# Kernel tuning notes

Hardware: AMD Instinct MI355X
Metric: run time of the kernel (lower is better)

The kernel has to match this reference:

```python
import jax, jax.numpy as jnp
import numpy as np

V, H, L, B = 32000, 1024, 2, 64
TEMP = 0.8


def setup_inputs() -> dict:
    key = jax.random.key(0)
    ks = jax.random.split(key, 12)
    sV = 1.0 / np.sqrt(V)
    sH = 1.0 / np.sqrt(H)
    return {
        "x": jax.random.normal(ks[0], (B, V), jnp.float32),
        "hidden_states": jax.random.normal(ks[1], (L, B, H), jnp.float32),
        "cell_states": jax.random.normal(ks[2], (L, B, H), jnp.float32),
        # gate order along axis 1: f, i, o, g
        "Wh": jax.random.uniform(ks[3], (L, 4, H, H), jnp.float32, -sH, sH),
        "bh": jax.random.uniform(ks[4], (L, 4, H), jnp.float32, -sH, sH),
        "Wx0": jax.random.uniform(ks[5], (4, H, V), jnp.float32, -sV, sV),
        "bx0": jax.random.uniform(ks[6], (4, H), jnp.float32, -sV, sV),
        "Wx1": jax.random.uniform(ks[7], (4, H, H), jnp.float32, -sH, sH),
        "bx1": jax.random.uniform(ks[8], (4, H), jnp.float32, -sH, sH),
        "Wdec": jax.random.uniform(ks[9], (V, H), jnp.float32, -sH, sH),
        "bdec": jax.random.uniform(ks[10], (V,), jnp.float32, -sH, sH),
    }


def _lstm_cell(inp, h, c, Wx, bx, Whl, bhl):
    # fused gate pre-activations: [B, 4, H]
    z = (jnp.einsum("ghk,bk->bgh", Wx, inp) + bx[None]
         + jnp.einsum("ghk,bk->bgh", Whl, h) + bhl[None])
    f = jax.nn.sigmoid(z[:, 0])
    i = jax.nn.sigmoid(z[:, 1])
    o = jax.nn.sigmoid(z[:, 2])
    g = jnp.tanh(z[:, 3])
    c_new = f * c + i * g
    out = o * jnp.tanh(c_new)
    return out, c_new


def reference(x, hidden_states, cell_states, Wh, bh, Wx0, bx0, Wx1, bx1, Wdec, bdec):
    wx = [(Wx0, bx0), (Wx1, bx1)]
    outputs, cstates = [], []
    inp = x
    for l in range(L):
        out, c_new = _lstm_cell(inp, hidden_states[l], cell_states[l],
                                wx[l][0], wx[l][1], Wh[l], bh[l])
        outputs.append(out)
        cstates.append(c_new)
        inp = out
    logits = outputs[-1] @ Wdec.T + bdec
    logp = jax.nn.log_softmax(logits / TEMP, axis=-1)
    return logp, jnp.stack(outputs), jnp.stack(cstates)
```

## Files before the change

### kernel.cpp

```cpp
#include <hip/hip_runtime.h>
#include <hip/hip_bf16.h>
#include <cstdint>

#define DI __device__ __forceinline__

typedef __attribute__((ext_vector_type(8))) short short8;
typedef __attribute__((ext_vector_type(4))) float f32x4;
typedef __attribute__((ext_vector_type(4))) int int4v;

DI f32x4 mfma16(short8 a, short8 b, f32x4 c) {
  return __builtin_amdgcn_mfma_f32_16x16x32_bf16(a, b, c, 0, 0, 0);
}

DI uint32_t f2bf(float f) {
  uint32_t u = __float_as_uint(f);
  return (u + 0x7fffu + ((u >> 16) & 1u)) >> 16;
}

DI uint32_t pk2(float a, float b) {
  return f2bf(a) | (f2bf(b) << 16);
}

DI short8 cvt8(float4 a, float4 b) {
  int4v t;
  t.x = (int)pk2(a.x, a.y);
  t.y = (int)pk2(a.z, a.w);
  t.z = (int)pk2(b.x, b.y);
  t.w = (int)pk2(b.z, b.w);
  return __builtin_bit_cast(short8, t);
}

__global__ __launch_bounds__(256) void convert_k(
    const float* __restrict__ x, const float* __restrict__ hs,
    ushort* __restrict__ xb, ushort* __restrict__ hb) {
  const int NX4 = 512000;
  const int NH4 = 32768;
  int i = blockIdx.x * 256 + threadIdx.x;
  if (i < NX4) {
    float4 v = *(const float4*)(x + 4 * (size_t)i);
    uint2 o;
    o.x = pk2(v.x, v.y);
    o.y = pk2(v.z, v.w);
    *(uint2*)(xb + 4 * (size_t)i) = o;
  } else if (i < NX4 + NH4) {
    int j = i - NX4;
    float4 v = *(const float4*)(hs + 4 * (size_t)j);
    uint2 o;
    o.x = pk2(v.x, v.y);
    o.y = pk2(v.z, v.w);
    *(uint2*)(hb + 4 * (size_t)j) = o;
  }
}

__global__ __launch_bounds__(256) void gemm_gates(
    const ushort* __restrict__ A1, const float* __restrict__ W1, int K1, int nch1, int steps1,
    const ushort* __restrict__ A2, const float* __restrict__ W2, int K2, int nch2, int steps2,
    float* __restrict__ zpart) {
  const int hblk = blockIdx.x;
  const int chunk = blockIdx.y;
  const ushort* A;
  const float* W;
  int K, steps;
  long kbase;
  if (chunk < nch1) {
    A = A1; W = W1; K = K1; steps = steps1;
    kbase = (long)chunk * steps1 * 32;
  } else {
    A = A2; W = W2; K = K2; steps = steps2;
    kbase = (long)(chunk - nch1) * steps2 * 32;
  }
  const int tid = threadIdx.x;
  const int wv = tid >> 6;
  const int lane = tid & 63;
  const int l15 = lane & 15;
  const int l4 = lane >> 4;
  const int h = hblk * 64 + wv * 16 + l15;

  const ushort* arow[4];
#pragma unroll
  for (int m = 0; m < 4; ++m)
    arow[m] = A + (size_t)(m * 16 + l15) * K + kbase + l4 * 8;
  const float* wrow[4];
#pragma unroll
  for (int g = 0; g < 4; ++g)
    wrow[g] = W + (size_t)(g * 1024 + h) * K + kbase + l4 * 8;

  f32x4 acc[4][4];
#pragma unroll
  for (int g = 0; g < 4; ++g)
#pragma unroll
    for (int m = 0; m < 4; ++m)
      acc[g][m] = f32x4{0.f, 0.f, 0.f, 0.f};

  for (int s = 0; s < steps; ++s) {
    short8 af[4];
#pragma unroll
    for (int m = 0; m < 4; ++m)
      af[m] = *(const short8*)(arow[m] + (size_t)s * 32);
#pragma unroll
    for (int g = 0; g < 4; ++g) {
      const float* wp = wrow[g] + (size_t)s * 32;
      float4 w0 = *(const float4*)wp;
      float4 w1 = *(const float4*)(wp + 4);
      short8 bfr = cvt8(w0, w1);
#pragma unroll
      for (int m = 0; m < 4; ++m)
        acc[g][m] = mfma16(af[m], bfr, acc[g][m]);
    }
  }

  float* zp = zpart + (size_t)chunk * (64 * 4096) + (size_t)(l4 * 4) * 4096 + h;
#pragma unroll
  for (int g = 0; g < 4; ++g)
#pragma unroll
    for (int m = 0; m < 4; ++m)
#pragma unroll
      for (int r = 0; r < 4; ++r)
        zp[(size_t)(m * 16 + r) * 4096 + g * 1024] = acc[g][m][r];
}

__global__ __launch_bounds__(256) void lstm_cell_k(
    const float* __restrict__ zpart, int nslots,
    const float* __restrict__ bx, const float* __restrict__ bhl,
    const float* __restrict__ c_in,
    float* __restrict__ h_out, float* __restrict__ c_out,
    ushort* __restrict__ h_out_b) {
  int idx = blockIdx.x * 256 + threadIdx.x;
  if (idx >= 64 * 1024) return;
  int h = idx & 1023;
  float z0 = bx[h] + bhl[h];
  float z1 = bx[1024 + h] + bhl[1024 + h];
  float z2 = bx[2048 + h] + bhl[2048 + h];
  float z3 = bx[3072 + h] + bhl[3072 + h];
  int b = idx >> 10;
  const float* zp = zpart + (size_t)b * 4096 + h;
  for (int s = 0; s < nslots; ++s) {
    const float* p = zp + (size_t)s * (64 * 4096);
    z0 += p[0];
    z1 += p[1024];
    z2 += p[2048];
    z3 += p[3072];
  }
  float f = 1.f / (1.f + expf(-z0));
  float i = 1.f / (1.f + expf(-z1));
  float o = 1.f / (1.f + expf(-z2));
  float g = tanhf(z3);
  float c = f * c_in[idx] + i * g;
  float hv = o * tanhf(c);
  h_out[idx] = hv;
  c_out[idx] = c;
  h_out_b[idx] = (ushort)f2bf(hv);
}

__global__ __launch_bounds__(256) void gemm_dec(
    const ushort* __restrict__ A, const float* __restrict__ W,
    const float* __restrict__ bias, float* __restrict__ logits) {
  const int nblk = blockIdx.x;
  const int tid = threadIdx.x;
  const int wv = tid >> 6;
  const int lane = tid & 63;
  const int l15 = lane & 15;
  const int l4 = lane >> 4;
  const int col = nblk * 64 + wv * 16 + l15;

  const ushort* arow[4];
#pragma unroll
  for (int m = 0; m < 4; ++m)
    arow[m] = A + (size_t)(m * 16 + l15) * 1024 + l4 * 8;
  const float* wrow = W + (size_t)col * 1024 + l4 * 8;

  f32x4 acc[4];
#pragma unroll
  for (int m = 0; m < 4; ++m) acc[m] = f32x4{0.f, 0.f, 0.f, 0.f};

  for (int s = 0; s < 32; ++s) {
    short8 af[4];
#pragma unroll
    for (int m = 0; m < 4; ++m)
      af[m] = *(const short8*)(arow[m] + (size_t)s * 32);
    const float* wp = wrow + (size_t)s * 32;
    float4 w0 = *(const float4*)wp;
    float4 w1 = *(const float4*)(wp + 4);
    short8 bfr = cvt8(w0, w1);
#pragma unroll
    for (int m = 0; m < 4; ++m)
      acc[m] = mfma16(af[m], bfr, acc[m]);
  }

  float bv = bias[col];
  float* lp = logits + (size_t)(l4 * 4) * 32000 + col;
#pragma unroll
  for (int m = 0; m < 4; ++m)
#pragma unroll
    for (int r = 0; r < 4; ++r)
      lp[(size_t)(m * 16 + r) * 32000] = acc[m][r] + bv;
}

__global__ __launch_bounds__(256) void softmax_k(
    const float* __restrict__ logits, float* __restrict__ logp) {
  const int b = blockIdx.x;
  const int tid = threadIdx.x;
  const int wv = tid >> 6;
  const int lane = tid & 63;
  const float* row = logits + (size_t)b * 32000;
  __shared__ float rbuf[4];

  float m = -1e30f;
  for (int i = tid; i < 32000; i += 256) m = fmaxf(m, row[i]);
#pragma unroll
  for (int d = 1; d < 64; d <<= 1) m = fmaxf(m, __shfl_xor(m, d));
  if (lane == 0) rbuf[wv] = m;
  __syncthreads();
  m = fmaxf(fmaxf(rbuf[0], rbuf[1]), fmaxf(rbuf[2], rbuf[3]));
  __syncthreads();

  float sum = 0.f;
  for (int i = tid; i < 32000; i += 256) sum += expf((row[i] - m) * 1.25f);
#pragma unroll
  for (int d = 1; d < 64; d <<= 1) sum += __shfl_xor(sum, d);
  if (lane == 0) rbuf[wv] = sum;
  __syncthreads();
  sum = rbuf[0] + rbuf[1] + rbuf[2] + rbuf[3];
  float lse = logf(sum);

  float* op = logp + (size_t)b * 32000;
  for (int i = tid; i < 32000; i += 256)
    op[i] = (row[i] - m) * 1.25f - lse;
}

extern "C" void kernel_launch(void* const* d_in, const int* in_sizes, int n_in,
                              void* d_out, int out_size, void* d_ws, size_t ws_size,
                              hipStream_t stream) {
  const float* x    = (const float*)d_in[0];
  const float* hs   = (const float*)d_in[1];
  const float* cs   = (const float*)d_in[2];
  const float* Wh   = (const float*)d_in[3];
  const float* bh   = (const float*)d_in[4];
  const float* Wx0  = (const float*)d_in[5];
  const float* bx0  = (const float*)d_in[6];
  const float* Wx1  = (const float*)d_in[7];
  const float* bx1  = (const float*)d_in[8];
  const float* Wdec = (const float*)d_in[9];
  const float* bdec = (const float*)d_in[10];

  float* out   = (float*)d_out;
  float* logp  = out;
  float* houts = out + 2048000;
  float* couts = out + 2179072;

  char* ws = (char*)d_ws;
  ushort* xb     = (ushort*)ws;
  ushort* hb     = (ushort*)(ws + 4096000);
  ushort* outb   = (ushort*)(ws + 4096000 + 262144);
  float*  logits = (float*)(ws + 4096000 + 262144 + 262144);
  float*  zpart  = (float*)(ws + 4096000 + 262144 + 262144 + 8192000);
  const size_t fixed = 4096000ull + 262144 + 262144 + 8192000;
  const size_t slot = (size_t)64 * 4096 * 4;

  int nch1 = 20, steps1 = 50;
  int l1ch = 8, l1steps = 4;
  if (fixed + 24 * slot > ws_size) {
    nch1 = 10; steps1 = 100;
    if (fixed + 16 * slot > ws_size) {
      nch1 = 4; steps1 = 250;
      l1ch = 4; l1steps = 8;
    }
  }

  convert_k<<<2128, 256, 0, stream>>>(x, hs, xb, hb);

  gemm_gates<<<dim3(16, nch1 + 4), 256, 0, stream>>>(
      xb, Wx0, 32000, nch1, steps1,
      hb, Wh, 1024, 4, 8, zpart);

  lstm_cell_k<<<256, 256, 0, stream>>>(zpart, nch1 + 4, bx0, bh, cs,
                                       houts, couts, outb);

  gemm_gates<<<dim3(16, 2 * l1ch), 256, 0, stream>>>(
      outb, Wx1, 1024, l1ch, l1steps,
      hb + 65536, Wh + 4194304, 1024, l1ch, l1steps, zpart);

  lstm_cell_k<<<256, 256, 0, stream>>>(zpart, 2 * l1ch, bx1, bh + 4096,
                                       cs + 65536, houts + 65536, couts + 65536,
                                       outb + 65536);

  gemm_dec<<<500, 256, 0, stream>>>(outb + 65536, Wdec, bdec, logits);

  softmax_k<<<64, 256, 0, stream>>>(logits, logp);
}
```

Before: 314.4 us.

## Split gate GEMM over gate axis, shrink decoder blocks, two-pass split softmax

The gate GEMM now launches one block per gate via a z grid dimension, so each block keeps a quarter of the accumulators. The layer-0 K-split also goes from 20 to 25 chunks. The decoder GEMM uses 64-thread blocks with four times as many blocks. The single-block-per-row softmax becomes two kernels: per-chunk max/sum partials, then a combine and write pass spread over more blocks. The aim is more parallelism and occupancy on the many CUs, at the cost of an extra launch, re-reading the logits, and reloading the A fragments once per gate.

```diff
diff --git a/kernel.cpp b/kernel.cpp
--- a/kernel.cpp
+++ b/kernel.cpp
@@ -58,6 +58,7 @@
     float* __restrict__ zpart) {
   const int hblk = blockIdx.x;
   const int chunk = blockIdx.y;
+  const int g = blockIdx.z;
   const ushort* A;
   const float* W;
   int K, steps;
@@ -80,43 +81,33 @@
 #pragma unroll
   for (int m = 0; m < 4; ++m)
     arow[m] = A + (size_t)(m * 16 + l15) * K + kbase + l4 * 8;
-  const float* wrow[4];
-#pragma unroll
-  for (int g = 0; g < 4; ++g)
-    wrow[g] = W + (size_t)(g * 1024 + h) * K + kbase + l4 * 8;
-
-  f32x4 acc[4][4];
-#pragma unroll
-  for (int g = 0; g < 4; ++g)
-#pragma unroll
-    for (int m = 0; m < 4; ++m)
-      acc[g][m] = f32x4{0.f, 0.f, 0.f, 0.f};
+  const float* wrow = W + (size_t)(g * 1024 + h) * K + kbase + l4 * 8;
+
+  f32x4 acc[4];
+#pragma unroll
+  for (int m = 0; m < 4; ++m) acc[m] = f32x4{0.f, 0.f, 0.f, 0.f};
 
   for (int s = 0; s < steps; ++s) {
     short8 af[4];
 #pragma unroll
     for (int m = 0; m < 4; ++m)
       af[m] = *(const short8*)(arow[m] + (size_t)s * 32);
-#pragma unroll
-    for (int g = 0; g < 4; ++g) {
-      const float* wp = wrow[g] + (size_t)s * 32;
-      float4 w0 = *(const float4*)wp;
-      float4 w1 = *(const float4*)(wp + 4);
-      short8 bfr = cvt8(w0, w1);
-#pragma unroll
-      for (int m = 0; m < 4; ++m)
-        acc[g][m] = mfma16(af[m], bfr, acc[g][m]);
-    }
-  }
-
-  float* zp = zpart + (size_t)chunk * (64 * 4096) + (size_t)(l4 * 4) * 4096 + h;
-#pragma unroll
-  for (int g = 0; g < 4; ++g)
-#pragma unroll
-    for (int m = 0; m < 4; ++m)
-#pragma unroll
-      for (int r = 0; r < 4; ++r)
-        zp[(size_t)(m * 16 + r) * 4096 + g * 1024] = acc[g][m][r];
+    const float* wp = wrow + (size_t)s * 32;
+    float4 w0 = *(const float4*)wp;
+    float4 w1 = *(const float4*)(wp + 4);
+    short8 bfr = cvt8(w0, w1);
+#pragma unroll
+    for (int m = 0; m < 4; ++m)
+      acc[m] = mfma16(af[m], bfr, acc[m]);
+  }
+
+  float* zp = zpart + (size_t)chunk * (64 * 4096) + (size_t)(l4 * 4) * 4096 +
+              g * 1024 + h;
+#pragma unroll
+  for (int m = 0; m < 4; ++m)
+#pragma unroll
+    for (int r = 0; r < 4; ++r)
+      zp[(size_t)(m * 16 + r) * 4096] = acc[m][r];
 }
 
 __global__ __launch_bounds__(256) void lstm_cell_k(
@@ -152,16 +143,13 @@
   h_out_b[idx] = (ushort)f2bf(hv);
 }
 
-__global__ __launch_bounds__(256) void gemm_dec(
+__global__ __launch_bounds__(64) void gemm_dec(
     const ushort* __restrict__ A, const float* __restrict__ W,
     const float* __restrict__ bias, float* __restrict__ logits) {
-  const int nblk = blockIdx.x;
-  const int tid = threadIdx.x;
-  const int wv = tid >> 6;
-  const int lane = tid & 63;
+  const int lane = threadIdx.x;
   const int l15 = lane & 15;
   const int l4 = lane >> 4;
-  const int col = nblk * 64 + wv * 16 + l15;
+  const int col = blockIdx.x * 16 + l15;
 
   const ushort* arow[4];
 #pragma unroll
@@ -196,17 +184,18 @@
       lp[(size_t)(m * 16 + r) * 32000] = acc[m][r] + bv;
 }
 
-__global__ __launch_bounds__(256) void softmax_k(
-    const float* __restrict__ logits, float* __restrict__ logp) {
-  const int b = blockIdx.x;
+__global__ __launch_bounds__(256) void softmax_part1(
+    const float* __restrict__ logits, float2* __restrict__ ms) {
+  const int cx = blockIdx.x;
+  const int b = blockIdx.y;
   const int tid = threadIdx.x;
   const int wv = tid >> 6;
   const int lane = tid & 63;
-  const float* row = logits + (size_t)b * 32000;
+  const float* row = logits + (size_t)b * 32000 + cx * 8000;
   __shared__ float rbuf[4];
 
   float m = -1e30f;
-  for (int i = tid; i < 32000; i += 256) m = fmaxf(m, row[i]);
+  for (int i = tid; i < 8000; i += 256) m = fmaxf(m, row[i]);
 #pragma unroll
   for (int d = 1; d < 64; d <<= 1) m = fmaxf(m, __shfl_xor(m, d));
   if (lane == 0) rbuf[wv] = m;
@@ -215,17 +204,35 @@
   __syncthreads();
 
   float sum = 0.f;
-  for (int i = tid; i < 32000; i += 256) sum += expf((row[i] - m) * 1.25f);
+  for (int i = tid; i < 8000; i += 256) sum += expf((row[i] - m) * 1.25f);
 #pragma unroll
   for (int d = 1; d < 64; d <<= 1) sum += __shfl_xor(sum, d);
   if (lane == 0) rbuf[wv] = sum;
   __syncthreads();
-  sum = rbuf[0] + rbuf[1] + rbuf[2] + rbuf[3];
-  float lse = logf(sum);
-
-  float* op = logp + (size_t)b * 32000;
-  for (int i = tid; i < 32000; i += 256)
-    op[i] = (row[i] - m) * 1.25f - lse;
+  if (tid == 0) {
+    sum = rbuf[0] + rbuf[1] + rbuf[2] + rbuf[3];
+    ms[b * 4 + cx] = make_float2(m, sum);
+  }
+}
+
+__global__ __launch_bounds__(256) void softmax_part2(
+    const float* __restrict__ logits, const float2* __restrict__ ms,
+    float* __restrict__ logp) {
+  const int cx = blockIdx.x;
+  const int b = blockIdx.y;
+  const int tid = threadIdx.x;
+
+  float2 p0 = ms[b * 4 + 0], p1 = ms[b * 4 + 1];
+  float2 p2 = ms[b * 4 + 2], p3 = ms[b * 4 + 3];
+  float M = fmaxf(fmaxf(p0.x, p1.x), fmaxf(p2.x, p3.x));
+  float S = p0.y * expf((p0.x - M) * 1.25f) + p1.y * expf((p1.x - M) * 1.25f) +
+            p2.y * expf((p2.x - M) * 1.25f) + p3.y * expf((p3.x - M) * 1.25f);
+  float lse = logf(S);
+
+  const float* row = logits + (size_t)b * 32000 + cx * 4000;
+  float* op = logp + (size_t)b * 32000 + cx * 4000;
+  for (int i = tid; i < 4000; i += 256)
+    op[i] = (row[i] - M) * 1.25f - lse;
 }
 
 extern "C" void kernel_launch(void* const* d_in, const int* in_sizes, int n_in,
@@ -253,13 +260,14 @@
   ushort* hb     = (ushort*)(ws + 4096000);
   ushort* outb   = (ushort*)(ws + 4096000 + 262144);
   float*  logits = (float*)(ws + 4096000 + 262144 + 262144);
-  float*  zpart  = (float*)(ws + 4096000 + 262144 + 262144 + 8192000);
-  const size_t fixed = 4096000ull + 262144 + 262144 + 8192000;
+  float2* ms     = (float2*)(ws + 4096000 + 262144 + 262144 + 8192000);
+  float*  zpart  = (float*)(ws + 4096000 + 262144 + 262144 + 8192000 + 2048);
+  const size_t fixed = 4096000ull + 262144 + 262144 + 8192000 + 2048;
   const size_t slot = (size_t)64 * 4096 * 4;
 
-  int nch1 = 20, steps1 = 50;
+  int nch1 = 25, steps1 = 40;
   int l1ch = 8, l1steps = 4;
-  if (fixed + 24 * slot > ws_size) {
+  if (fixed + 29 * slot > ws_size) {
     nch1 = 10; steps1 = 100;
     if (fixed + 16 * slot > ws_size) {
       nch1 = 4; steps1 = 250;
@@ -269,14 +277,14 @@
 
   convert_k<<<2128, 256, 0, stream>>>(x, hs, xb, hb);
 
-  gemm_gates<<<dim3(16, nch1 + 4), 256, 0, stream>>>(
+  gemm_gates<<<dim3(16, nch1 + 4, 4), 256, 0, stream>>>(
       xb, Wx0, 32000, nch1, steps1,
       hb, Wh, 1024, 4, 8, zpart);
 
   lstm_cell_k<<<256, 256, 0, stream>>>(zpart, nch1 + 4, bx0, bh, cs,
                                        houts, couts, outb);
 
-  gemm_gates<<<dim3(16, 2 * l1ch), 256, 0, stream>>>(
+  gemm_gates<<<dim3(16, 2 * l1ch, 4), 256, 0, stream>>>(
       outb, Wx1, 1024, l1ch, l1steps,
       hb + 65536, Wh + 4194304, 1024, l1ch, l1steps, zpart);
 
@@ -284,7 +292,8 @@
                                        cs + 65536, houts + 65536, couts + 65536,
                                        outb + 65536);
 
-  gemm_dec<<<500, 256, 0, stream>>>(outb + 65536, Wdec, bdec, logits);
-
-  softmax_k<<<64, 256, 0, stream>>>(logits, logp);
-}
+  gemm_dec<<<2000, 64, 0, stream>>>(outb + 65536, Wdec, bdec, logits);
+
+  softmax_part1<<<dim3(4, 64), 256, 0, stream>>>(logits, ms);
+  softmax_part2<<<dim3(8, 64), 256, 0, stream>>>(logits, ms, logp);
+}
```

New measurement: 346.1 us. 10.1% more time.
